# Performance work log

Measured on AMD Instinct MI355X. Metric: run time of the kernel, lower is better.

The kernel has to match this reference:

```python
import jax, jax.numpy as jnp
import numpy as np

N_NODES = 100_000
E_OFF = 1_500_000
LATENT = 64
MP_STEPS = 3


def setup_inputs() -> dict:
    key = jax.random.key(0)
    ks = jax.random.split(key, 12)
    # lower-triangular graph: all self-loops + random off-diagonal edges with row >= col
    r = jax.random.randint(ks[0], (E_OFF,), 0, N_NODES)
    c = jax.random.randint(ks[1], (E_OFF,), 0, N_NODES)
    diag = jnp.arange(N_NODES)
    edge_row = jnp.concatenate([jnp.maximum(r, c), diag]).astype(jnp.int64)
    edge_col = jnp.concatenate([jnp.minimum(r, c), diag]).astype(jnp.int64)
    E = E_OFF + N_NODES
    # positive weights (gcn_norm takes deg^{-1/2} of weighted degree)
    edge_attr = jax.random.uniform(ks[2], (E,), jnp.float32) + 0.05
    x = jax.random.normal(ks[3], (N_NODES, 1), jnp.float32)
    L = LATENT
    def lin(k, fi, fo):
        return jax.random.normal(k, (fi, fo), jnp.float32) / np.sqrt(fi)
    return {
        "x": x,
        "edge_attr": edge_attr,
        "w_enc": lin(ks[4], 1, L), "b_enc": jnp.zeros((L,), jnp.float32),
        "conv1_w": jax.random.normal(ks[5], (MP_STEPS, L, L), jnp.float32) / np.sqrt(L),
        "conv1_b": jnp.zeros((MP_STEPS, L), jnp.float32),
        "conv2_w": jax.random.normal(ks[6], (MP_STEPS, L, L), jnp.float32) / np.sqrt(L),
        "conv2_b": jnp.zeros((MP_STEPS, L), jnp.float32),
        "dec_w1": lin(ks[7], 2 * L, L), "dec_b1": jnp.zeros((L,), jnp.float32),
        "dec_w2": lin(ks[8], L, 1), "dec_b2": jnp.zeros((1,), jnp.float32),
        "edge_row": edge_row,
        "edge_col": edge_col,
    }


def reference(x, edge_attr, w_enc, b_enc, conv1_w, conv1_b, conv2_w, conv2_b,
              dec_w1, dec_b1, dec_w2, dec_b2, edge_row, edge_col):
    N = x.shape[0]
    # GCN normalization (graph already contains all self-loops, so PyG's
    # add_remaining_self_loops is a no-op and keeps existing loop weights)
    deg = jax.ops.segment_sum(edge_attr, edge_col, num_segments=N)
    dinv = jnp.where(deg > 0, jax.lax.rsqrt(jnp.maximum(deg, 1e-30)), 0.0)
    norm = dinv[edge_row] * edge_attr * dinv[edge_col]  # [E]
    cnt = jnp.maximum(
        jax.ops.segment_sum(jnp.ones_like(edge_attr), edge_col, num_segments=N), 1.0
    )[:, None]  # mean aggregation denominator

    def gcn(h, W, b):
        m = (h @ W)[edge_row] * norm[:, None]           # [E, F] messages
        agg = jax.ops.segment_sum(m, edge_col, num_segments=N) / cnt
        return agg + b

    # node encoder: single Linear (no activation)
    h = x @ w_enc + b_enc
    for i in range(MP_STEPS):
        h = jax.nn.relu(gcn(h, conv1_w[i], conv1_b[i]))
        h = jax.nn.relu(gcn(h, conv2_w[i], conv2_b[i]))

    # edge decoder: gather endpoints, MLP [2L -> L -> 1]
    e = jnp.concatenate([h[edge_row], h[edge_col]], axis=1)
    e = jax.nn.relu(e @ dec_w1 + dec_b1)
    e = (e @ dec_w2 + dec_b2)[:, 0]                      # [E]
    vals = jnp.where(edge_row == edge_col, jax.nn.softplus(e), e)
    return vals
```

## Files before the change

### kernel.cpp

```cpp
#include <hip/hip_runtime.h>
#include <hip/hip_fp16.h>
#include <math.h>

#define L 64
#define FIXS 65536.0f
#define WAITCNT_LGKM0 0xC07F

#define FMAMIX_LO(acc, pkh, ws) \
    asm("v_fma_mix_f32 %0, %1, %2, %0 op_sel:[0,0,0] op_sel_hi:[1,0,0]" \
        : "+v"(acc) : "v"(pkh), "v"(ws))
#define FMAMIX_HI(acc, pkh, ws) \
    asm("v_fma_mix_f32 %0, %1, %2, %0 op_sel:[1,0,0] op_sel_hi:[1,0,0]" \
        : "+v"(acc) : "v"(pkh), "v"(ws))
#define PKADDRELU(d, a, b) \
    asm("v_pk_add_f16 %0, %1, %2\n\tv_pk_max_f16 %0, %0, 0" \
        : "=v"(d) : "v"(a), "v"(b))

#define GLOAD(xw_, qv_, J) \
    xw_ = (unsigned)__shfl((int)mwv, (J) * 8 + grp); \
    qv_ = h4[(size_t)(xw_ & 0x1FFFFu) * 8 + sub];
#define FMA8(A, qv_, xw_) { \
    float wv_ = __half2float(__ushort_as_half((unsigned short)((xw_) >> 17))); \
    FMAMIX_LO(A[0], (qv_).x, wv_); FMAMIX_HI(A[1], (qv_).x, wv_); \
    FMAMIX_LO(A[2], (qv_).y, wv_); FMAMIX_HI(A[3], (qv_).y, wv_); \
    FMAMIX_LO(A[4], (qv_).z, wv_); FMAMIX_HI(A[5], (qv_).z, wv_); \
    FMAMIX_LO(A[6], (qv_).w, wv_); FMAMIX_HI(A[7], (qv_).w, wv_); }


__global__ void k_hist(const int* __restrict__ col, const float* __restrict__ attr,
                       unsigned* __restrict__ degcnt,
                       int* __restrict__ rank, int E) {
    int e = blockIdx.x * blockDim.x + threadIdx.x;
    if (e < E) {
        int c = col[e];
        unsigned fx = (unsigned)(int)rintf(attr[e] * FIXS);
        unsigned old = atomicAdd(&degcnt[c], (1u << 24) | fx);
        rank[e] = (int)(old >> 24);
    }
}

__global__ void k_dinv(const unsigned* __restrict__ degcnt,
                       float* __restrict__ dinv, int* __restrict__ cntI,
                       float* __restrict__ rcnt, int N) {
    int n = blockIdx.x * blockDim.x + threadIdx.x;
    if (n < N) {
        unsigned p = degcnt[n];
        unsigned cnt = p >> 24;
        float d = (float)(p & 0xFFFFFFu) * (1.0f / FIXS);
        dinv[n] = (d > 0.f) ? (1.0f / sqrtf(fmaxf(d, 1e-30f))) : 0.f;
        cntI[n] = (int)cnt;
        unsigned c = cnt ? cnt : 1u;
        rcnt[n] = 1.0f / (float)c;
    }
}


__global__ __launch_bounds__(256) void k_scan_a(const int* __restrict__ cntI,
                                                int* __restrict__ blockSums, int N) {
    __shared__ int red[4];
    int b = blockIdx.x, t = threadIdx.x;
    int base = b * 1024 + t * 4;
    int s = 0;
    #pragma unroll
    for (int i = 0; i < 4; ++i) { int idx = base + i; if (idx < N) s += cntI[idx]; }
    #pragma unroll
    for (int off = 32; off > 0; off >>= 1) s += __shfl_down(s, off);
    if ((t & 63) == 0) red[t >> 6] = s;
    __syncthreads();
    if (t == 0) blockSums[b] = red[0] + red[1] + red[2] + red[3];
}

__global__ __launch_bounds__(1024) void k_scan_b(int* __restrict__ blockSums, int B,
                                                 int* __restrict__ ptr, int N) {
    __shared__ int sh[1024];
    int t = threadIdx.x;
    sh[t] = (t < B) ? blockSums[t] : 0;
    __syncthreads();
    for (int off = 1; off < 1024; off <<= 1) {
        int v = (t >= off) ? sh[t - off] : 0;
        __syncthreads();
        sh[t] += v;
        __syncthreads();
    }
    if (t < B) blockSums[t] = (t == 0) ? 0 : sh[t - 1];
    if (t == B - 1) ptr[N] = sh[t];
}

__global__ __launch_bounds__(256) void k_scan_c(const int* __restrict__ cntI,
                                                const int* __restrict__ blockSums,
                                                int* __restrict__ ptr, int N) {
    __shared__ int th[256];
    int b = blockIdx.x, t = threadIdx.x;
    int base = b * 1024 + t * 4;
    int v[4]; int s = 0;
    #pragma unroll
    for (int i = 0; i < 4; ++i) {
        int idx = base + i;
        v[i] = (idx < N) ? cntI[idx] : 0;
        s += v[i];
    }
    th[t] = s;
    __syncthreads();
    for (int off = 1; off < 256; off <<= 1) {
        int xv = (t >= off) ? th[t - off] : 0;
        __syncthreads();
        th[t] += xv;
        __syncthreads();
    }
    int pre = ((t == 0) ? 0 : th[t - 1]) + blockSums[b];
    #pragma unroll
    for (int i = 0; i < 4; ++i) {
        int idx = base + i;
        if (idx < N) ptr[idx] = pre;
        pre += v[i];
    }
}

__global__ void k_scatter(const int* __restrict__ row, const int* __restrict__ col,
                          const float* __restrict__ attr, const float* __restrict__ dinv,
                          const int* __restrict__ colptr,
                          int* __restrict__ rank,
                          unsigned* __restrict__ csrX, int* __restrict__ colof, int E) {
    int e = blockIdx.x * blockDim.x + threadIdx.x;
    if (e < E) {
        int r = row[e], c = col[e];
        int pos = colptr[c] + rank[e];
        float nrm = dinv[r] * attr[e] * dinv[c];
        unsigned short nb = __half_as_ushort(__float2half(nrm));
        csrX[pos] = (unsigned)r | ((unsigned)nb << 17);
        colof[pos] = c;
        rank[e] = pos;
    }
}


__global__ void k_encode(const float* __restrict__ x, const float* __restrict__ w_enc,
                         const float* __restrict__ b_enc, __half* __restrict__ h, int N) {
    int idx = blockIdx.x * blockDim.x + threadIdx.x;
    if (idx < N * L) {
        int n = idx >> 6, f = idx & 63;
        h[idx] = __float2half(x[n] * w_enc[f] + b_enc[f]);
    }
}


__global__ __launch_bounds__(256, 4) void k_gcn(const uint4* __restrict__ h4,
        __half* __restrict__ h_out,
        const float* __restrict__ W, const float* __restrict__ bias,
        const int* __restrict__ colptr, const unsigned* __restrict__ csrX,
        const float* __restrict__ rcnt, int N) {
    __shared__ float sm[4][72];
    int lane = threadIdx.x & 63;
    int warp = threadIdx.x >> 6;
    int grp  = lane >> 3;
    int sub  = lane & 7;
    int wid  = (blockIdx.x * blockDim.x + threadIdx.x) >> 6;
    int nw   = (gridDim.x * blockDim.x) >> 6;
    float* smw = &sm[warp][0];

    float Wc[L];
    #pragma unroll
    for (int f = 0; f < L; ++f) Wc[f] = W[f * L + lane];
    float bl = bias[lane];

    int beg = 0, end = 0; unsigned mw = 0;
    if (wid < N) {
        beg = colptr[wid];
        end = colptr[wid + 1];
        if (beg + lane < end) mw = csrX[beg + lane];
    }

    for (int n = wid; n < N; n += nw) {
        int n2 = n + nw;
        int beg2 = 0, end2 = 0;
        if (n2 < N) { beg2 = colptr[n2]; end2 = colptr[n2 + 1]; }
        float rcv = rcnt[n];

        float va[8], vb[8];
        #pragma unroll
        for (int i = 0; i < 8; ++i) { va[i] = 0.f; vb[i] = 0.f; }

        auto PROC = [&](unsigned mwv, int mm) {
            int kmax = (mm + 7) >> 3;
            int k = 0;
            while (k < kmax) {
                int rem = kmax - k;
                if (rem >= 4) {
                    unsigned x0, x1, x2, x3; uint4 q0, q1, q2, q3;
                    GLOAD(x0, q0, k) GLOAD(x1, q1, k + 1)
                    GLOAD(x2, q2, k + 2) GLOAD(x3, q3, k + 3)
                    FMA8(va, q0, x0) FMA8(vb, q1, x1)
                    FMA8(va, q2, x2) FMA8(vb, q3, x3)
                    k += 4;
                } else if (rem == 3) {
                    unsigned x0, x1, x2; uint4 q0, q1, q2;
                    GLOAD(x0, q0, k) GLOAD(x1, q1, k + 1) GLOAD(x2, q2, k + 2)
                    FMA8(va, q0, x0) FMA8(vb, q1, x1) FMA8(va, q2, x2)
                    k += 3;
                } else if (rem == 2) {
                    unsigned x0, x1; uint4 q0, q1;
                    GLOAD(x0, q0, k) GLOAD(x1, q1, k + 1)
                    FMA8(va, q0, x0) FMA8(vb, q1, x1)
                    k += 2;
                } else {
                    unsigned x0; uint4 q0;
                    GLOAD(x0, q0, k)
                    FMA8(va, q0, x0)
                    k += 1;
                }
            }
        };

        int m = end - beg; if (m > 64) m = 64;
        PROC(mw, m);
        for (int base = beg + 64; base < end; base += 64) {
            int mm = end - base; if (mm > 64) mm = 64;
            unsigned mwc = 0;
            if (lane < mm) mwc = csrX[base + lane];
            PROC(mwc, mm);
        }

        unsigned mw2 = 0;
        if (n2 < N && beg2 + lane < end2) mw2 = csrX[beg2 + lane];

        float s[8];
        #pragma unroll
        for (int i = 0; i < 8; ++i) {
            float v = va[i] + vb[i];
            v += __shfl_xor(v, 8);
            v += __shfl_xor(v, 16);
            v += __shfl_xor(v, 32);
            s[i] = v;
        }
        if (lane < 8) {
            #pragma unroll
            for (int i = 0; i < 8; ++i) smw[8 * lane + i] = s[i];
        }
        __builtin_amdgcn_s_waitcnt(WAITCNT_LGKM0);
        float a0 = 0.f, a1 = 0.f, a2 = 0.f, a3 = 0.f;
        const float4* smv = (const float4*)smw;
        #pragma unroll
        for (int q = 0; q < 16; ++q) {
            float4 sv = smv[q];
            a0 += sv.x * Wc[4 * q + 0];
            a1 += sv.y * Wc[4 * q + 1];
            a2 += sv.z * Wc[4 * q + 2];
            a3 += sv.w * Wc[4 * q + 3];
        }
        float o = ((a0 + a1) + (a2 + a3)) * rcv + bl;
        h_out[(size_t)n * L + lane] = __float2half(fmaxf(o, 0.f));

        beg = beg2; end = end2; mw = mw2;
    }
}


__global__ __launch_bounds__(256, 2) void k_mv2(const __half* __restrict__ h,
        const float* __restrict__ W1, const float* __restrict__ b1,
        __half* __restrict__ U, __half* __restrict__ V, int N) {
    __shared__ float sm[4][72];
    int lane = threadIdx.x & 63;
    int warp = threadIdx.x >> 6;
    int wid  = (blockIdx.x * blockDim.x + threadIdx.x) >> 6;
    int nw   = (gridDim.x * blockDim.x) >> 6;
    float* smw = &sm[warp][0];
    float Wu[L], Wv[L];
    #pragma unroll
    for (int f = 0; f < L; ++f) Wu[f] = W1[f * L + lane];
    #pragma unroll
    for (int f = 0; f < L; ++f) Wv[f] = W1[(L + f) * L + lane];
    float bl = b1[lane];
    for (int n = wid; n < N; n += nw) {
        float hl = __half2float(h[(size_t)n * L + lane]);
        smw[lane] = hl;
        __builtin_amdgcn_s_waitcnt(WAITCNT_LGKM0);
        float a0 = 0.f, a1 = 0.f, c0 = 0.f, c1 = 0.f;
        const float4* smv = (const float4*)smw;
        #pragma unroll
        for (int q = 0; q < 16; ++q) {
            float4 sv = smv[q];
            a0 += sv.x * Wu[4 * q + 0] ; a1 += sv.y * Wu[4 * q + 1];
            a0 += sv.z * Wu[4 * q + 2] ; a1 += sv.w * Wu[4 * q + 3];
            c0 += sv.x * Wv[4 * q + 0] ; c1 += sv.y * Wv[4 * q + 1];
            c0 += sv.z * Wv[4 * q + 2] ; c1 += sv.w * Wv[4 * q + 3];
        }
        U[(size_t)n * L + lane] = __float2half((a0 + a1) + bl);
        V[(size_t)n * L + lane] = __float2half(c0 + c1);
        __builtin_amdgcn_s_waitcnt(WAITCNT_LGKM0);
    }
}


__global__ __launch_bounds__(256, 8) void k_edge(const __half* __restrict__ U,
        const __half* __restrict__ V, const float* __restrict__ w2,
        const float* __restrict__ b2, const unsigned* __restrict__ csrX,
        const int* __restrict__ colof, float* __restrict__ tmp, int E) {
    int sub = threadIdx.x & 7;
    float w2f[8];
    #pragma unroll
    for (int i = 0; i < 8; ++i) w2f[i] = w2[8 * sub + i];
    float b2v = b2[0];
    int tid = blockIdx.x * blockDim.x + threadIdx.x;
    int np  = (gridDim.x * blockDim.x) >> 3;
    for (int p = tid >> 3; p < E; p += np) {
        unsigned md = csrX[p];
        int r = (int)(md & 0x1FFFFu);
        int n = colof[p];
        uint4 uq = ((const uint4*)(U + (size_t)r * L))[sub];
        uint4 vq = ((const uint4*)(V + (size_t)n * L))[sub];
        float p0 = 0.f, p1 = 0.f;
        #define DOT2X(uw_, vw_, B) { unsigned t_; \
            PKADDRELU(t_, (uw_), (vw_)); \
            FMAMIX_LO(p0, t_, w2f[B]); FMAMIX_HI(p1, t_, w2f[(B) + 1]); }
        DOT2X(uq.x, vq.x, 0) DOT2X(uq.y, vq.y, 2)
        DOT2X(uq.z, vq.z, 4) DOT2X(uq.w, vq.w, 6)
        #undef DOT2X
        float pd = p0 + p1;
        pd += __shfl_xor(pd, 1);
        pd += __shfl_xor(pd, 2);
        pd += __shfl_xor(pd, 4);
        if (sub == 0) tmp[p] = pd + b2v;
    }
}


__global__ void k_perm(const int* __restrict__ epos, const float* __restrict__ tmp,
                       const int* __restrict__ erow, const int* __restrict__ ecol,
                       float* __restrict__ out, int E) {
    int e = blockIdx.x * blockDim.x + threadIdx.x;
    if (e < E) {
        float val = tmp[epos[e]];
        if (erow[e] == ecol[e])
            val = fmaxf(val, 0.f) + log1pf(expf(-fabsf(val)));
        out[e] = val;
    }
}


extern "C" void kernel_launch(void* const* d_in, const int* in_sizes, int n_in,
                              void* d_out, int out_size, void* d_ws, size_t ws_size,
                              hipStream_t stream) {
    const float* x     = (const float*)d_in[0];
    const float* attr  = (const float*)d_in[1];
    const float* w_enc = (const float*)d_in[2];
    const float* b_enc = (const float*)d_in[3];
    const float* c1w   = (const float*)d_in[4];
    const float* c1b   = (const float*)d_in[5];
    const float* c2w   = (const float*)d_in[6];
    const float* c2b   = (const float*)d_in[7];
    const float* dw1   = (const float*)d_in[8];
    const float* db1   = (const float*)d_in[9];
    const float* dw2   = (const float*)d_in[10];
    const float* db2   = (const float*)d_in[11];
    const int*   erow  = (const int*)d_in[12];
    const int*   ecol  = (const int*)d_in[13];
    int N = in_sizes[0];
    int E = in_sizes[1];
    float* out = (float*)d_out;

    char* w = (char*)d_ws;
    auto alloc = [&](size_t bytes) {
        char* p = w; w += (bytes + 255) & ~(size_t)255; return p;
    };
    unsigned* degcnt = (unsigned*)alloc((size_t)N * 4);
    size_t zbytes = (size_t)(w - (char*)d_ws);
    float* dinv   = (float*)alloc((size_t)N * 4);
    int*   cntI   = (int*)  alloc((size_t)N * 4);
    float* rcnt   = (float*)alloc((size_t)N * 4);
    int*   colptr = (int*)  alloc((size_t)(N + 1) * 4);
    int*   bsums  = (int*)  alloc(((size_t)(N + 1023) / 1024 + 1) * 4);
    int*   rank   = (int*)  alloc((size_t)E * 4);
    unsigned* csrX = (unsigned*)alloc((size_t)E * 4);
    int*   colof  = (int*)  alloc((size_t)E * 4);
    float* tmp    = (float*)alloc((size_t)E * 4);
    __half* hA    = (__half*)alloc((size_t)N * L * 2);
    __half* hB    = (__half*)alloc((size_t)N * L * 2);
    __half* hU    = (__half*)alloc((size_t)N * L * 2);
    __half* hV    = (__half*)alloc((size_t)N * L * 2);
    (void)ws_size; (void)n_in; (void)out_size;

    (void)hipMemsetAsync(d_ws, 0, zbytes, stream);

    int eb = (E + 255) / 256;
    int nb = (N + 255) / 256;
    int B  = (N + 1023) / 1024;
    k_hist<<<eb, 256, 0, stream>>>(ecol, attr, degcnt, rank, E);
    k_dinv<<<nb, 256, 0, stream>>>(degcnt, dinv, cntI, rcnt, N);
    k_scan_a<<<B, 256, 0, stream>>>(cntI, bsums, N);
    k_scan_b<<<1, 1024, 0, stream>>>(bsums, B, colptr, N);
    k_scan_c<<<B, 256, 0, stream>>>(cntI, bsums, colptr, N);
    k_scatter<<<eb, 256, 0, stream>>>(erow, ecol, attr, dinv, colptr, rank,
                                      csrX, colof, E);
    k_encode<<<(N * L + 255) / 256, 256, 0, stream>>>(x, w_enc, b_enc, hA, N);

    __half* hin = hA; __half* hout = hB;
    for (int i = 0; i < 3; ++i) {
        k_gcn<<<2048, 256, 0, stream>>>((const uint4*)hin, hout, c1w + i * L * L,
                                        c1b + i * L, colptr, csrX, rcnt, N);
        __half* t = hin; hin = hout; hout = t;
        k_gcn<<<2048, 256, 0, stream>>>((const uint4*)hin, hout, c2w + i * L * L,
                                        c2b + i * L, colptr, csrX, rcnt, N);
        t = hin; hin = hout; hout = t;
    }
    k_mv2<<<2048, 256, 0, stream>>>(hin, dw1, db1, hU, hV, N);
    k_edge<<<2048, 256, 0, stream>>>(hU, hV, dw2, db2, csrX, colof, tmp, E);
    k_perm<<<eb, 256, 0, stream>>>(rank, tmp, erow, ecol, out, E);
}
```

Measured before the change: 634.8 us.

## Fill CSR column index with coalesced per-node kernel; single accumulator in GCN

Removes the random scattered write of colof from k_scatter and adds a k_fill kernel that writes each node's column index contiguously over its CSR range, replacing random stores with coalesced ones. In k_gcn the dual accumulators va/vb are merged into one, cutting register use, and the launch bound minimum blocks per CU is relaxed from 4 to 2. The single accumulator lengthens the FMA dependency chain, and the looser launch bound may let the compiler use more registers and lower occupancy for this latency-bound gather.

```diff
diff --git a/kernel.cpp b/kernel.cpp
--- a/kernel.cpp
+++ b/kernel.cpp
@@ -120,7 +120,7 @@
                           const float* __restrict__ attr, const float* __restrict__ dinv,
                           const int* __restrict__ colptr,
                           int* __restrict__ rank,
-                          unsigned* __restrict__ csrX, int* __restrict__ colof, int E) {
+                          unsigned* __restrict__ csrX, int E) {
     int e = blockIdx.x * blockDim.x + threadIdx.x;
     if (e < E) {
         int r = row[e], c = col[e];
@@ -128,8 +128,19 @@
         float nrm = dinv[r] * attr[e] * dinv[c];
         unsigned short nb = __half_as_ushort(__float2half(nrm));
         csrX[pos] = (unsigned)r | ((unsigned)nb << 17);
-        colof[pos] = c;
         rank[e] = pos;
+    }
+}
+
+
+__global__ __launch_bounds__(256) void k_fill(const int* __restrict__ colptr,
+                                              int* __restrict__ colof, int N) {
+    int lane = threadIdx.x & 63;
+    int wid  = (blockIdx.x * blockDim.x + threadIdx.x) >> 6;
+    int nw   = (gridDim.x * blockDim.x) >> 6;
+    for (int n = wid; n < N; n += nw) {
+        int beg = colptr[n], end = colptr[n + 1];
+        for (int p = beg + lane; p < end; p += 64) colof[p] = n;
     }
 }
 
@@ -144,7 +155,7 @@
 }
 
 
-__global__ __launch_bounds__(256, 4) void k_gcn(const uint4* __restrict__ h4,
+__global__ __launch_bounds__(256, 2) void k_gcn(const uint4* __restrict__ h4,
         __half* __restrict__ h_out,
         const float* __restrict__ W, const float* __restrict__ bias,
         const int* __restrict__ colptr, const unsigned* __restrict__ csrX,
@@ -176,9 +187,9 @@
         if (n2 < N) { beg2 = colptr[n2]; end2 = colptr[n2 + 1]; }
         float rcv = rcnt[n];
 
-        float va[8], vb[8];
+        float va[8];
         #pragma unroll
-        for (int i = 0; i < 8; ++i) { va[i] = 0.f; vb[i] = 0.f; }
+        for (int i = 0; i < 8; ++i) va[i] = 0.f;
 
         auto PROC = [&](unsigned mwv, int mm) {
             int kmax = (mm + 7) >> 3;
@@ -189,18 +200,18 @@
                     unsigned x0, x1, x2, x3; uint4 q0, q1, q2, q3;
                     GLOAD(x0, q0, k) GLOAD(x1, q1, k + 1)
                     GLOAD(x2, q2, k + 2) GLOAD(x3, q3, k + 3)
-                    FMA8(va, q0, x0) FMA8(vb, q1, x1)
-                    FMA8(va, q2, x2) FMA8(vb, q3, x3)
+                    FMA8(va, q0, x0) FMA8(va, q1, x1)
+                    FMA8(va, q2, x2) FMA8(va, q3, x3)
                     k += 4;
                 } else if (rem == 3) {
                     unsigned x0, x1, x2; uint4 q0, q1, q2;
                     GLOAD(x0, q0, k) GLOAD(x1, q1, k + 1) GLOAD(x2, q2, k + 2)
-                    FMA8(va, q0, x0) FMA8(vb, q1, x1) FMA8(va, q2, x2)
+                    FMA8(va, q0, x0) FMA8(va, q1, x1) FMA8(va, q2, x2)
                     k += 3;
                 } else if (rem == 2) {
                     unsigned x0, x1; uint4 q0, q1;
                     GLOAD(x0, q0, k) GLOAD(x1, q1, k + 1)
-                    FMA8(va, q0, x0) FMA8(vb, q1, x1)
+                    FMA8(va, q0, x0) FMA8(va, q1, x1)
                     k += 2;
                 } else {
                     unsigned x0; uint4 q0;
@@ -226,7 +237,7 @@
         float s[8];
         #pragma unroll
         for (int i = 0; i < 8; ++i) {
-            float v = va[i] + vb[i];
+            float v = va[i];
             v += __shfl_xor(v, 8);
             v += __shfl_xor(v, 16);
             v += __shfl_xor(v, 32);
@@ -389,8 +400,8 @@
     k_scan_a<<<B, 256, 0, stream>>>(cntI, bsums, N);
     k_scan_b<<<1, 1024, 0, stream>>>(bsums, B, colptr, N);
     k_scan_c<<<B, 256, 0, stream>>>(cntI, bsums, colptr, N);
-    k_scatter<<<eb, 256, 0, stream>>>(erow, ecol, attr, dinv, colptr, rank,
-                                      csrX, colof, E);
+    k_scatter<<<eb, 256, 0, stream>>>(erow, ecol, attr, dinv, colptr, rank, csrX, E);
+    k_fill<<<1024, 256, 0, stream>>>(colptr, colof, N);
     k_encode<<<(N * L + 255) / 256, 256, 0, stream>>>(x, w_enc, b_enc, hA, N);
 
     __half* hin = hA; __half* hout = hB;
```

Measured after the change: 636.6 us. About the same (+0.3%).
